# Optimization experiments

Measured on AMD Instinct MI355X. Metric: run time of the kernel, lower is better.

The kernel has to match this reference:

```python
import jax, jax.numpy as jnp
import numpy as np

B, S, E, H, MAXLEN = 2, 2048, 1024, 16, 2048


def _level_indices(seq_len: int, base: int = 2) -> np.ndarray:
    """Vectorized version of get_level_index_weak over the full (target, source) grid.
    indices[t, s] = min(level, 2) for s < t, else 0. Runs in O(log S) passes."""
    tt = np.broadcast_to(np.arange(seq_len)[:, None], (seq_len, seq_len)).astype(np.int64).copy()
    ss = np.broadcast_to(np.arange(seq_len)[None, :], (seq_len, seq_len)).astype(np.int64).copy()
    res = np.zeros((seq_len, seq_len), np.int64)
    done = ~(ss < tt)  # only source < target positions get a level; rest stay 0
    while not done.all():
        l = np.floor(np.log2(np.maximum(tt, 1).astype(np.float64))).astype(np.int64)
        v = (np.int64(1) << l)
        hit = (~done) & (ss < v)
        res[hit] = l[hit] + 1
        done |= hit
        step = ~done
        tt[step] -= v[step]
        ss[step] -= v[step]
    return np.minimum(res, 2).astype(np.int32)


def setup_inputs() -> dict:
    key = jax.random.key(0)
    ks = jax.random.split(key, 10)
    sc = 0.02
    return {
        "x": jax.random.normal(ks[0], (B, S, E), dtype=jnp.float32),
        "attention_mask": jax.random.randint(ks[1], (B, S), 0, 2, dtype=jnp.int32),
        "level_indices": jnp.asarray(_level_indices(S, 2)),
        "Wq": jax.random.normal(ks[2], (E, E), dtype=jnp.float32) * sc,
        "bq": jnp.zeros((E,), jnp.float32),
        "Wk": jax.random.normal(ks[3], (E, E), dtype=jnp.float32) * sc,
        "bk": jnp.zeros((E,), jnp.float32),
        "Wv": jax.random.normal(ks[4], (E, E), dtype=jnp.float32) * sc,
        "bv": jnp.zeros((E,), jnp.float32),
        "hier": jax.random.normal(ks[5], (MAXLEN, H, 3), dtype=jnp.float32),
        "Wo": jax.random.normal(ks[6], (E, E), dtype=jnp.float32) * sc,
        "bo": jnp.zeros((E,), jnp.float32),
    }


def reference(x, attention_mask, level_indices, Wq, bq, Wk, bk, Wv, bv, hier, Wo, bo):
    b, s, e = x.shape
    h = hier.shape[1]
    dh = e // h
    # q/k are computed by the original module but never used; kept for fidelity (zero grads).
    q = x @ Wq.T + bq
    k = x @ Wk.T + bk
    v = (x @ Wv.T + bv).reshape(b, s, h, dh).transpose(0, 2, 1, 3)  # [B,H,S,Dh]
    lev = level_indices[:s, :s]  # [S,S] int, values in {0,1,2}
    # Faithful torch.gather semantics: weights[b,h,i,j] = hier[b, h, lev[i,j]]
    w3 = hier[:b]                      # [B,H,3]
    weights = w3[:, :, lev]            # [B,H,S,S]
    decay = jnp.power(jnp.float32(0.5), lev.astype(x.dtype))  # [S,S]
    weights = weights * decay
    weights = weights / (jnp.sum(weights, axis=-1, keepdims=True) + 1e-8)
    weights = jnp.where(attention_mask[:, None, None, :] == 0, jnp.float32(0.0), weights)
    out = jnp.einsum('bhij,bhjd->bhid', weights, v)  # [B,H,S,Dh]
    out = out.transpose(0, 2, 1, 3).reshape(b, s, e)
    return out @ Wo.T + bo
```

## Files before the change

kernel.cpp:

```cpp
#include <hip/hip_runtime.h>
#include <cstdint>
#include <cstddef>

constexpr int Sn = 2048;
constexpr int En = 1024;
constexpr int Bn = 2;
constexpr int Hn = 16;
constexpr int NCH = 32;
constexpr int CHUNK = 64;

typedef __bf16 bf16x8 __attribute__((ext_vector_type(8)));
typedef float  f32x4  __attribute__((ext_vector_type(4)));

#define GLOBAL_AS(p) ((const __attribute__((address_space(1))) void*)(p))
#define LDS_AS(p)    ((__attribute__((address_space(3))) void*)(p))

__device__ __forceinline__ unsigned short f2bf(float f) {
    union { float f; uint32_t u; } v; v.f = f;
    const uint32_t u = v.u;
    return (unsigned short)((u + 0x7fffu + ((u >> 16) & 1u)) >> 16);
}
__device__ __forceinline__ float bf2f_lo(uint32_t u) {
    union { uint32_t u; float f; } v; v.u = u << 16; return v.f;
}
__device__ __forceinline__ float bf2f_hi(uint32_t u) {
    union { uint32_t u; float f; } v; v.u = u & 0xffff0000u; return v.f;
}

constexpr int XN = Bn * Sn * En;
constexpr int WN = En * En;

__global__ __launch_bounds__(256)
void cast3(const float* __restrict__ x, const float* __restrict__ Wv,
           const float* __restrict__ Wo, unsigned short* __restrict__ xb,
           unsigned short* __restrict__ Wvb, unsigned short* __restrict__ Wob)
{
    const int i = (blockIdx.x * 256 + threadIdx.x) * 4;
    const float* src; unsigned short* dst; int off;
    if (i < XN)           { src = x;  dst = xb;  off = i; }
    else if (i < XN + WN) { src = Wv; dst = Wvb; off = i - XN; }
    else                  { src = Wo; dst = Wob; off = i - XN - WN; }
    const float4 v = *(const float4*)(src + off);
    ushort4 o;
    o.x = f2bf(v.x); o.y = f2bf(v.y); o.z = f2bf(v.z); o.w = f2bf(v.w);
    *(ushort4*)(dst + off) = o;
}

template<bool APPLY_MASK, bool OUT_BF16>
__global__ __launch_bounds__(256)
void gemm_mfma(const unsigned short* __restrict__ A, const unsigned short* __restrict__ Bw,
               const float* __restrict__ bias, const int* __restrict__ mask,
               void* __restrict__ Cv, int M, int N, int K)
{
    __shared__ __align__(16) unsigned short As[128 * 32];
    __shared__ __align__(16) unsigned short Bs[64 * 32];

    const int tid  = threadIdx.x;
    const int lane = tid & 63;
    const int wv   = tid >> 6;
    const int wr   = wv >> 1;
    const int wc   = wv & 1;
    const int bm   = blockIdx.y * 128;
    const int bn   = blockIdx.x * 64;
    const int m16  = lane & 15;
    const int kq   = lane >> 4;

    f32x4 acc[4][2] = {};

    const int j0 = 2 * wv, j1 = 2 * wv + 1;
    const unsigned short* gA0 = A  + (size_t)(bm + 16 * j0 + m16) * K + kq * 8;
    const unsigned short* gA1 = A  + (size_t)(bm + 16 * j1 + m16) * K + kq * 8;
    const unsigned short* gB0 = Bw + (size_t)(bn + 16 * wv + m16) * K + kq * 8;
    unsigned short* lA0 = &As[j0 * 512];
    unsigned short* lA1 = &As[j1 * 512];
    unsigned short* lB0 = &Bs[wv * 512];

    for (int k0 = 0; k0 < K; k0 += 32) {
        __syncthreads();
        __builtin_amdgcn_global_load_lds(GLOBAL_AS(gA0 + k0), LDS_AS(lA0), 16, 0, 0);
        __builtin_amdgcn_global_load_lds(GLOBAL_AS(gA1 + k0), LDS_AS(lA1), 16, 0, 0);
        __builtin_amdgcn_global_load_lds(GLOBAL_AS(gB0 + k0), LDS_AS(lB0), 16, 0, 0);
        __syncthreads();

        bf16x8 af[4], bfr[2];
#pragma unroll
        for (int i = 0; i < 4; ++i)
            af[i] = *(const bf16x8*)&As[(wr * 4 + i) * 512 + lane * 8];
#pragma unroll
        for (int j = 0; j < 2; ++j)
            bfr[j] = *(const bf16x8*)&Bs[(wc * 2 + j) * 512 + lane * 8];
#pragma unroll
        for (int i = 0; i < 4; ++i)
#pragma unroll
            for (int j = 0; j < 2; ++j)
                acc[i][j] = __builtin_amdgcn_mfma_f32_16x16x32_bf16(af[i], bfr[j], acc[i][j], 0, 0, 0);
    }

#pragma unroll
    for (int i = 0; i < 4; ++i) {
        const int r0 = bm + wr * 64 + i * 16 + kq * 4;
#pragma unroll
        for (int j = 0; j < 2; ++j) {
            const int c0 = bn + wc * 32 + j * 16 + m16;
            const float bcol = bias[c0];
#pragma unroll
            for (int r = 0; r < 4; ++r) {
                const int row = r0 + r;
                float val = acc[i][j][r] + bcol;
                if (APPLY_MASK) val = (mask[row] == 0) ? 0.0f : val;
                if (OUT_BF16)
                    ((unsigned short*)Cv)[(size_t)row * N + c0] = f2bf(val);
                else
                    ((float*)Cv)[(size_t)row * N + c0] = val;
            }
        }
    }
}

__global__ __launch_bounds__(256)
void chunk_sum(const unsigned short* __restrict__ vm, float* __restrict__ csum)
{
    const int ep = blockIdx.x * 256 + threadIdx.x;
    const int e = ep * 2;
    const int c = blockIdx.y;
    const int b = blockIdx.z;
    const size_t base = ((size_t)b * Sn + c * CHUNK) * En + e;
    float s0 = 0.0f, s1 = 0.0f;
    for (int t = 0; t < CHUNK; ++t) {
        const uint32_t u = *(const uint32_t*)(vm + base + (size_t)t * En);
        s0 += bf2f_lo(u);
        s1 += bf2f_hi(u);
    }
    const size_t o = ((size_t)b * NCH + c) * En + e;
    csum[o] = s0;
    csum[o + 1] = s1;
}

__global__ __launch_bounds__(256)
void chunk_scan(const float* __restrict__ csum, float* __restrict__ cscan,
                float* __restrict__ Tbuf)
{
    const int idx = blockIdx.x * 256 + threadIdx.x;
    const int b = idx >> 10;
    const int e = idx & (En - 1);
    float run = 0.0f;
    for (int c = 0; c < NCH; ++c) {
        const size_t off = ((size_t)b * NCH + c) * En + e;
        const float v = csum[off];
        cscan[off] = run;
        run += v;
    }
    Tbuf[idx] = run;
}

__global__ __launch_bounds__(256)
void combine(const unsigned short* __restrict__ vm, const float* __restrict__ cscan,
             const float* __restrict__ Tbuf, const float* __restrict__ hier,
             unsigned short* __restrict__ opre)
{
    const int ep = blockIdx.x * 256 + threadIdx.x;
    const int e = ep * 2;
    const int c = blockIdx.y;
    const int b = blockIdx.z;
    const int h = e >> 6;

    const float w0 = hier[((size_t)b * Hn + h) * 3 + 0];
    const float w1 = hier[((size_t)b * Hn + h) * 3 + 1] * 0.5f;
    const float w2 = hier[((size_t)b * Hn + h) * 3 + 2] * 0.25f;
    const float T0 = Tbuf[(size_t)b * En + e];
    const float T1 = Tbuf[(size_t)b * En + e + 1];

    const size_t co = ((size_t)b * NCH + c) * En + e;
    float run0 = cscan[co], run1 = cscan[co + 1];
    float prev0 = 0.0f, prev1 = 0.0f;
    const size_t base = ((size_t)b * Sn + c * CHUNK) * En + e;

    for (int t = 0; t < CHUNK; ++t) {
        const int i = c * CHUNK + t;
        const uint32_t u = *(const uint32_t*)(vm + base + (size_t)t * En);
        const float cur0 = bf2f_lo(u), cur1 = bf2f_hi(u);
        float num0, num1, Z;
        if (i & 1) {
            num0 = w2 * (run0 - prev0) + w1 * prev0 + w0 * (T0 - run0);
            num1 = w2 * (run1 - prev1) + w1 * prev1 + w0 * (T1 - run1);
            Z = (float)(i - 1) * w2 + w1 + (float)(Sn - i) * w0 + 1e-8f;
        } else {
            num0 = w2 * run0 + w0 * (T0 - run0);
            num1 = w2 * run1 + w0 * (T1 - run1);
            Z = (float)i * w2 + (float)(Sn - i) * w0 + 1e-8f;
        }
        const float rz = 1.0f / Z;
        const uint32_t o = (uint32_t)f2bf(num0 * rz) | ((uint32_t)f2bf(num1 * rz) << 16);
        *(uint32_t*)(opre + base + (size_t)t * En) = o;
        run0 += cur0; run1 += cur1;
        prev0 = cur0; prev1 = cur1;
    }
}

extern "C" void kernel_launch(void* const* d_in, const int* in_sizes, int n_in,
                              void* d_out, int out_size, void* d_ws, size_t ws_size,
                              hipStream_t stream)
{
    const float* x    = (const float*)d_in[0];
    const int*   mask = (const int*)d_in[1];
    const float* Wv   = (const float*)d_in[7];
    const float* bv   = (const float*)d_in[8];
    const float* hier = (const float*)d_in[9];
    const float* Wo   = (const float*)d_in[10];
    const float* bo   = (const float*)d_in[11];
    float* out = (float*)d_out;

    const int M = Bn * Sn, N = En, K = En;

    char* ws = (char*)d_ws;
    unsigned short* xb    = (unsigned short*)ws;  ws += (size_t)M * K * 2;
    unsigned short* Wvb   = (unsigned short*)ws;  ws += (size_t)N * K * 2;
    unsigned short* Wob   = (unsigned short*)ws;  ws += (size_t)N * K * 2;
    unsigned short* vmb   = (unsigned short*)ws;  ws += (size_t)M * N * 2;
    float*          csum  = (float*)ws;           ws += (size_t)Bn * NCH * En * 4;
    float*          cscan = (float*)ws;           ws += (size_t)Bn * NCH * En * 4;
    float*          Tbuf  = (float*)ws;           ws += (size_t)Bn * En * 4;
    unsigned short* opreb = (unsigned short*)ws;  ws += (size_t)M * N * 2;

    dim3 threads(256);

    cast3<<<dim3((XN + 2 * WN) / 1024), threads, 0, stream>>>(x, Wv, Wo, xb, Wvb, Wob);

    dim3 gemm_grid(N / 64, M / 128);

    gemm_mfma<true, true><<<gemm_grid, threads, 0, stream>>>(xb, Wvb, bv, mask, vmb, M, N, K);
    chunk_sum<<<dim3(En / 512, NCH, Bn), threads, 0, stream>>>(vmb, csum);
    chunk_scan<<<dim3((Bn * En) / 256), threads, 0, stream>>>(csum, cscan, Tbuf);
    combine<<<dim3(En / 512, NCH, Bn), threads, 0, stream>>>(vmb, cscan, Tbuf, hier, opreb);
    gemm_mfma<false, false><<<gemm_grid, threads, 0, stream>>>(opreb, Wob, bo, nullptr, out, M, N, K);
}
```

Baseline: 177.8 us.

## Fuse chunk column sums into V GEMM epilogue and deepen GEMM K-tile

The per-chunk column sums that the separate chunk_sum kernel used to compute are now accumulated in the V-projection GEMM epilogue. Each wave sums its 64 output rows, reduces across lanes with shuffles and writes csum directly. This removes one kernel launch and a full re-read of the bf16 V matrix. The GEMM K-step also grows from 32 to 64, which halves the number of barrier and load rounds at the cost of doubled LDS tiles and more fragment registers. The sums now use unrounded fp32 values instead of the bf16-stored ones, so results can differ slightly.

```diff
diff --git a/kernel.cpp b/kernel.cpp
--- a/kernel.cpp
+++ b/kernel.cpp
@@ -46,14 +46,14 @@
     *(ushort4*)(dst + off) = o;
 }
 
-template<bool APPLY_MASK, bool OUT_BF16>
+template<bool APPLY_MASK, bool OUT_BF16, bool FUSE_CSUM>
 __global__ __launch_bounds__(256)
 void gemm_mfma(const unsigned short* __restrict__ A, const unsigned short* __restrict__ Bw,
                const float* __restrict__ bias, const int* __restrict__ mask,
-               void* __restrict__ Cv, int M, int N, int K)
-{
-    __shared__ __align__(16) unsigned short As[128 * 32];
-    __shared__ __align__(16) unsigned short Bs[64 * 32];
+               void* __restrict__ Cv, float* __restrict__ csum, int M, int N, int K)
+{
+    __shared__ __align__(16) unsigned short As[128 * 64];
+    __shared__ __align__(16) unsigned short Bs[64 * 64];
 
     const int tid  = threadIdx.x;
     const int lane = tid & 63;
@@ -71,31 +71,44 @@
     const unsigned short* gA0 = A  + (size_t)(bm + 16 * j0 + m16) * K + kq * 8;
     const unsigned short* gA1 = A  + (size_t)(bm + 16 * j1 + m16) * K + kq * 8;
     const unsigned short* gB0 = Bw + (size_t)(bn + 16 * wv + m16) * K + kq * 8;
-    unsigned short* lA0 = &As[j0 * 512];
-    unsigned short* lA1 = &As[j1 * 512];
-    unsigned short* lB0 = &Bs[wv * 512];
-
-    for (int k0 = 0; k0 < K; k0 += 32) {
+    unsigned short* lA00 = &As[(j0 * 2 + 0) * 512];
+    unsigned short* lA01 = &As[(j0 * 2 + 1) * 512];
+    unsigned short* lA10 = &As[(j1 * 2 + 0) * 512];
+    unsigned short* lA11 = &As[(j1 * 2 + 1) * 512];
+    unsigned short* lB00 = &Bs[(wv * 2 + 0) * 512];
+    unsigned short* lB01 = &Bs[(wv * 2 + 1) * 512];
+
+    for (int k0 = 0; k0 < K; k0 += 64) {
         __syncthreads();
-        __builtin_amdgcn_global_load_lds(GLOBAL_AS(gA0 + k0), LDS_AS(lA0), 16, 0, 0);
-        __builtin_amdgcn_global_load_lds(GLOBAL_AS(gA1 + k0), LDS_AS(lA1), 16, 0, 0);
-        __builtin_amdgcn_global_load_lds(GLOBAL_AS(gB0 + k0), LDS_AS(lB0), 16, 0, 0);
+        __builtin_amdgcn_global_load_lds(GLOBAL_AS(gA0 + k0),      LDS_AS(lA00), 16, 0, 0);
+        __builtin_amdgcn_global_load_lds(GLOBAL_AS(gA0 + k0 + 32), LDS_AS(lA01), 16, 0, 0);
+        __builtin_amdgcn_global_load_lds(GLOBAL_AS(gA1 + k0),      LDS_AS(lA10), 16, 0, 0);
+        __builtin_amdgcn_global_load_lds(GLOBAL_AS(gA1 + k0 + 32), LDS_AS(lA11), 16, 0, 0);
+        __builtin_amdgcn_global_load_lds(GLOBAL_AS(gB0 + k0),      LDS_AS(lB00), 16, 0, 0);
+        __builtin_amdgcn_global_load_lds(GLOBAL_AS(gB0 + k0 + 32), LDS_AS(lB01), 16, 0, 0);
         __syncthreads();
 
-        bf16x8 af[4], bfr[2];
+        bf16x8 af[4][2], bfr[2][2];
 #pragma unroll
         for (int i = 0; i < 4; ++i)
-            af[i] = *(const bf16x8*)&As[(wr * 4 + i) * 512 + lane * 8];
+#pragma unroll
+            for (int kk = 0; kk < 2; ++kk)
+                af[i][kk] = *(const bf16x8*)&As[((wr * 4 + i) * 2 + kk) * 512 + lane * 8];
 #pragma unroll
         for (int j = 0; j < 2; ++j)
-            bfr[j] = *(const bf16x8*)&Bs[(wc * 2 + j) * 512 + lane * 8];
-#pragma unroll
-        for (int i = 0; i < 4; ++i)
-#pragma unroll
-            for (int j = 0; j < 2; ++j)
-                acc[i][j] = __builtin_amdgcn_mfma_f32_16x16x32_bf16(af[i], bfr[j], acc[i][j], 0, 0, 0);
-    }
-
+#pragma unroll
+            for (int kk = 0; kk < 2; ++kk)
+                bfr[j][kk] = *(const bf16x8*)&Bs[((wc * 2 + j) * 2 + kk) * 512 + lane * 8];
+#pragma unroll
+        for (int kk = 0; kk < 2; ++kk)
+#pragma unroll
+            for (int i = 0; i < 4; ++i)
+#pragma unroll
+                for (int j = 0; j < 2; ++j)
+                    acc[i][j] = __builtin_amdgcn_mfma_f32_16x16x32_bf16(af[i][kk], bfr[j][kk], acc[i][j], 0, 0, 0);
+    }
+
+    float colsum[2] = {0.0f, 0.0f};
 #pragma unroll
     for (int i = 0; i < 4; ++i) {
         const int r0 = bm + wr * 64 + i * 16 + kq * 4;
@@ -108,6 +121,7 @@
                 const int row = r0 + r;
                 float val = acc[i][j][r] + bcol;
                 if (APPLY_MASK) val = (mask[row] == 0) ? 0.0f : val;
+                if (FUSE_CSUM) colsum[j] += val;
                 if (OUT_BF16)
                     ((unsigned short*)Cv)[(size_t)row * N + c0] = f2bf(val);
                 else
@@ -115,25 +129,18 @@
             }
         }
     }
-}
-
-__global__ __launch_bounds__(256)
-void chunk_sum(const unsigned short* __restrict__ vm, float* __restrict__ csum)
-{
-    const int ep = blockIdx.x * 256 + threadIdx.x;
-    const int e = ep * 2;
-    const int c = blockIdx.y;
-    const int b = blockIdx.z;
-    const size_t base = ((size_t)b * Sn + c * CHUNK) * En + e;
-    float s0 = 0.0f, s1 = 0.0f;
-    for (int t = 0; t < CHUNK; ++t) {
-        const uint32_t u = *(const uint32_t*)(vm + base + (size_t)t * En);
-        s0 += bf2f_lo(u);
-        s1 += bf2f_hi(u);
-    }
-    const size_t o = ((size_t)b * NCH + c) * En + e;
-    csum[o] = s0;
-    csum[o + 1] = s1;
+
+    if (FUSE_CSUM) {
+        const int gc = 2 * blockIdx.y + wr;
+#pragma unroll
+        for (int j = 0; j < 2; ++j) {
+            float s = colsum[j];
+            s += __shfl_xor(s, 16, 64);
+            s += __shfl_xor(s, 32, 64);
+            if (kq == 0)
+                csum[(size_t)gc * En + bn + wc * 32 + j * 16 + m16] = s;
+        }
+    }
 }
 
 __global__ __launch_bounds__(256)
@@ -141,9 +148,9 @@
                 float* __restrict__ Tbuf)
 {
     const int idx = blockIdx.x * 256 + threadIdx.x;
+    float run = 0.0f;
     const int b = idx >> 10;
     const int e = idx & (En - 1);
-    float run = 0.0f;
     for (int c = 0; c < NCH; ++c) {
         const size_t off = ((size_t)b * NCH + c) * En + e;
         const float v = csum[off];
@@ -228,9 +235,8 @@
 
     dim3 gemm_grid(N / 64, M / 128);
 
-    gemm_mfma<true, true><<<gemm_grid, threads, 0, stream>>>(xb, Wvb, bv, mask, vmb, M, N, K);
-    chunk_sum<<<dim3(En / 512, NCH, Bn), threads, 0, stream>>>(vmb, csum);
+    gemm_mfma<true, true, true><<<gemm_grid, threads, 0, stream>>>(xb, Wvb, bv, mask, vmb, csum, M, N, K);
     chunk_scan<<<dim3((Bn * En) / 256), threads, 0, stream>>>(csum, cscan, Tbuf);
     combine<<<dim3(En / 512, NCH, Bn), threads, 0, stream>>>(vmb, cscan, Tbuf, hier, opreb);
-    gemm_mfma<false, false><<<gemm_grid, threads, 0, stream>>>(opreb, Wob, bo, nullptr, out, M, N, K);
-}
+    gemm_mfma<false, false, false><<<gemm_grid, threads, 0, stream>>>(opreb, Wob, bo, nullptr, out, nullptr, M, N, K);
+}
```

After: 172.3 us. -3.1%, faster.
